# Kernel tuning notes

Hardware: AMD Instinct MI355X
Metric: run time of the kernel (lower is better)

The kernel has to match this reference:

```python
import jax, jax.numpy as jnp
import numpy as np

HIDDEN = 1024
NUM_HEADS = 16
HEAD_DIM = HIDDEN // NUM_HEADS
B, S = 2, 2048


def setup_inputs() -> dict:
    key = jax.random.key(0)
    ks = jax.random.split(key, 7)
    scale = 1.0 / np.sqrt(HIDDEN)
    return {
        "hidden_states": jax.random.normal(ks[0], (B, S, HIDDEN), dtype=jnp.float32),
        "attention_mask": jnp.ones((B, S), dtype=jnp.float32),
        "Wq": jax.random.normal(ks[1], (HIDDEN, HIDDEN), dtype=jnp.float32) * scale,
        "bq": jax.random.normal(ks[2], (HIDDEN,), dtype=jnp.float32) * 0.02,
        "Wk": jax.random.normal(ks[3], (HIDDEN, HIDDEN), dtype=jnp.float32) * scale,
        "bk": jax.random.normal(ks[4], (HIDDEN,), dtype=jnp.float32) * 0.02,
        "Wv": jax.random.normal(ks[5], (HIDDEN, HIDDEN), dtype=jnp.float32) * scale,
        "bv": jax.random.normal(ks[6], (HIDDEN,), dtype=jnp.float32) * 0.02,
    }


def reference(hidden_states, attention_mask, Wq, bq, Wk, bk, Wv, bv):
    # Linear projections (W stored [in, out], equivalent to torch Linear).
    q = hidden_states @ Wq + bq  # [B,S,H]
    k = hidden_states @ Wk + bk
    v = hidden_states @ Wv + bv

    def split_heads(x):  # [B,S,H] -> [B,nh,S,hd]
        return x.reshape(B, S, NUM_HEADS, HEAD_DIM).transpose(0, 2, 1, 3)

    q, k, v = split_heads(q), split_heads(k), split_heads(v)

    scores = jnp.einsum("bhqd,bhkd->bhqk", q, k) / jnp.sqrt(
        jnp.asarray(HEAD_DIM, dtype=q.dtype))
    min_val = jnp.finfo(scores.dtype).min
    ext_mask = (1.0 - attention_mask[:, None, None, :]) * min_val  # [B,1,1,S]
    scores = scores + ext_mask
    probs = jax.nn.softmax(scores, axis=-1)  # eval mode: no dropout
    ctx = jnp.einsum("bhqk,bhkd->bhqd", probs, v)
    ctx = ctx.transpose(0, 2, 1, 3).reshape(B, S, HIDDEN)
    return ctx
```

## Files before the change

kernel.cpp:

```cpp
#include <hip/hip_runtime.h>
#include <hip/hip_bf16.h>
#include <cstddef>
#include <cstdint>

#define HID 1024
#define NHEADS 16
#define HDIM 64
#define BATCH 2
#define SEQ 2048
#define MROWS (BATCH * SEQ)
#define BHT (BATCH * NHEADS)

typedef __attribute__((ext_vector_type(8))) short s8v;
typedef __attribute__((ext_vector_type(4))) float f4v;

__device__ __forceinline__ unsigned short f2bf(float x) {
    union { float f; unsigned int u; } c; c.f = x;
    return (unsigned short)((c.u + 0x7fffu + ((c.u >> 16) & 1u)) >> 16);
}
__device__ __forceinline__ unsigned int pkbf(float a, float b) {
    __hip_bfloat162 h = __float22bfloat162_rn(float2{a, b});
    union { __hip_bfloat162 v; unsigned int u; } c; c.v = h; return c.u;
}
__device__ __forceinline__ float bflo(unsigned int w) {
    union { unsigned int u; float f; } c; c.u = w << 16; return c.f;
}
__device__ __forceinline__ float bfhi(unsigned int w) {
    union { unsigned int u; float f; } c; c.u = w & 0xffff0000u; return c.f;
}

__device__ __forceinline__ void lds_load16(void* lds, const void* g) {
    __builtin_amdgcn_global_load_lds(
        (const __attribute__((address_space(1))) void*)g,
        (__attribute__((address_space(3))) void*)lds, 16, 0, 0);
}

__global__ __launch_bounds__(256) void conv_hs_kernel(
    const float* __restrict__ hs, unsigned short* __restrict__ Ah)
{
    const int idx = (blockIdx.x * 256 + threadIdx.x) * 4;
    float4 v = *(const float4*)&hs[idx];
    union { unsigned int w[2]; unsigned long long q; } pk;
    pk.w[0] = pkbf(v.x, v.y);
    pk.w[1] = pkbf(v.z, v.w);
    *(unsigned long long*)&Ah[idx] = pk.q;
}

__global__ __launch_bounds__(256) void conv_wt_kernel(
    const float* __restrict__ Wq, const float* __restrict__ Wk,
    const float* __restrict__ Wv, unsigned short* __restrict__ WTh)
{
    const int z = blockIdx.z;
    const float* W = (z == 0) ? Wq : (z == 1) ? Wk : Wv;
    unsigned short* th = WTh + (size_t)z * HID * HID;

    __shared__ float tile[64][65];
    const int t = threadIdx.x;
    const int kb = blockIdx.y * 64, nb = blockIdx.x * 64;
    const int c4 = (t & 15) * 4;
    const int r0 = t >> 4;

#pragma unroll
    for (int i = 0; i < 4; ++i) {
        int r = r0 + i * 16;
        float4 v = *(const float4*)&W[(size_t)(kb + r) * HID + nb + c4];
        tile[r][c4 + 0] = v.x; tile[r][c4 + 1] = v.y;
        tile[r][c4 + 2] = v.z; tile[r][c4 + 3] = v.w;
    }
    __syncthreads();
#pragma unroll
    for (int i = 0; i < 4; ++i) {
        int n = r0 + i * 16;
        union { unsigned int w[2]; unsigned long long q; } pk;
        pk.w[0] = pkbf(tile[c4 + 0][n], tile[c4 + 1][n]);
        pk.w[1] = pkbf(tile[c4 + 2][n], tile[c4 + 3][n]);
        *(unsigned long long*)&th[(size_t)(nb + n) * HID + kb + c4] = pk.q;
    }
}

#define GBM 128
#define GBN 128
#define QSCALE 0.18033688011112042f

__global__ __launch_bounds__(256) void qkv_mfma_kernel(
    const unsigned short* __restrict__ Ah, const unsigned short* __restrict__ WTh,
    const float* __restrict__ bq, const float* __restrict__ bk,
    const float* __restrict__ bv,
    unsigned short* __restrict__ Qg, unsigned short* __restrict__ Khi,
    unsigned short* __restrict__ VTg)
{
    const int z = blockIdx.z;
    const float* bias = (z == 0) ? bq : (z == 1) ? bk : bv;
    const unsigned short* Bh = WTh + (size_t)z * HID * HID;

    __shared__ unsigned short AS[GBM * 64];
    __shared__ unsigned short BS[GBN * 64];

    const int t = threadIdx.x;
    const int wave = t >> 6, lane = t & 63, quad = lane >> 4, l15 = lane & 15;
    const int sw = l15 & 7;
    const int wm = wave >> 1, wn = wave & 1;
    const int rowBase = blockIdx.x * GBM;
    const int colBase = blockIdx.y * GBN;

    const int srow8 = lane >> 3;
    const int sc    = lane & 7;

    f4v acc[4][4];
#pragma unroll
    for (int mf = 0; mf < 4; ++mf)
#pragma unroll
        for (int nf = 0; nf < 4; ++nf) acc[mf][nf] = (f4v){0.f, 0.f, 0.f, 0.f};

    for (int kt = 0; kt < HID / 64; ++kt) {
        const int k0 = kt * 64;
        __syncthreads();
#pragma unroll
        for (int it = 0; it < 4; ++it) {
            const int i = wave * 4 + it;
            const int row = i * 8 + srow8;
            const int gx = (sc ^ (row & 7)) * 8;
            lds_load16(&AS[i * 512], &Ah[(size_t)(rowBase + row) * HID + k0 + gx]);
            lds_load16(&BS[i * 512], &Bh[(size_t)(colBase + row) * HID + k0 + gx]);
        }
        __syncthreads();

#pragma unroll
        for (int kk = 0; kk < 2; ++kk) {
            s8v af[4], bf[4];
#pragma unroll
            for (int mf = 0; mf < 4; ++mf)
                af[mf] = *(const s8v*)&AS[(wm * 64 + mf * 16 + l15) * 64 + (((kk * 4 + quad) ^ sw) * 8)];
#pragma unroll
            for (int nf = 0; nf < 4; ++nf)
                bf[nf] = *(const s8v*)&BS[(wn * 64 + nf * 16 + l15) * 64 + (((kk * 4 + quad) ^ sw) * 8)];
#pragma unroll
            for (int mf = 0; mf < 4; ++mf)
#pragma unroll
                for (int nf = 0; nf < 4; ++nf)
                    acc[mf][nf] = __builtin_amdgcn_mfma_f32_16x16x32_bf16(af[mf], bf[nf], acc[mf][nf], 0, 0, 0);
        }
    }

#pragma unroll
    for (int nf = 0; nf < 4; ++nf) {
        const int n = colBase + wn * 64 + nf * 16 + l15;
        const float bb = bias[n];
        const int h = n >> 6, d = n & 63;
#pragma unroll
        for (int mf = 0; mf < 4; ++mf) {
            const int rw0 = rowBase + wm * 64 + mf * 16 + quad * 4;
            const int b = rw0 >> 11;
            const int s0 = rw0 & (SEQ - 1);
            float c[4];
#pragma unroll
            for (int r = 0; r < 4; ++r) c[r] = acc[mf][nf][r] + bb;
            if (z == 0) {
#pragma unroll
                for (int r = 0; r < 4; ++r) {
                    const size_t base = ((size_t)(b * NHEADS + h) * SEQ + s0 + r) * HDIM + d;
                    Qg[base] = f2bf(c[r] * QSCALE);
                }
            } else if (z == 1) {
#pragma unroll
                for (int r = 0; r < 4; ++r) {
                    const size_t base = ((size_t)(b * NHEADS + h) * SEQ + s0 + r) * HDIM + d;
                    Khi[base] = f2bf(c[r]);
                }
            } else {
                union { unsigned int w[2]; unsigned long long q; } pk;
                pk.w[0] = pkbf(c[0], c[1]);
                pk.w[1] = pkbf(c[2], c[3]);
                *(unsigned long long*)&VTg[((size_t)(b * NHEADS + h) * HDIM + d) * SEQ + s0] = pk.q;
            }
        }
    }
}

#define BC 64

__global__ __launch_bounds__(256, 2) void attn_mfma_kernel(
    const unsigned short* __restrict__ Qg, const unsigned short* __restrict__ Khi,
    const unsigned short* __restrict__ VTg,
    const float* __restrict__ mask, float* __restrict__ out)
{
    __shared__ unsigned short Kb[2][BC * HDIM];
    __shared__ unsigned short Vb[2][BC * HDIM];
    __shared__ unsigned short Pbuf[4][32 * BC];

    const int t = threadIdx.x;
    const int wave = t >> 6, lane = t & 63, quad = lane >> 4, l15 = lane & 15;
    const int sw = l15 & 7;
    const int bh = blockIdx.x, b = bh >> 4, h = bh & (NHEADS - 1);
    const int qbase = blockIdx.y * 128 + wave * 32;

    const size_t hb = (size_t)bh * SEQ * HDIM;
    const unsigned short* kbase = Khi + hb;
    const unsigned short* vbase = VTg + hb;
    const float* mrow = mask + b * SEQ;

    s8v qh[2][2];
#pragma unroll
    for (int qf = 0; qf < 2; ++qf)
#pragma unroll
        for (int ds = 0; ds < 2; ++ds) {
            size_t off = hb + (size_t)(qbase + qf * 16 + l15) * HDIM + ds * 32 + quad * 8;
            qh[qf][ds] = *(const s8v*)&Qg[off];
        }

    f4v oacc[2][4];
#pragma unroll
    for (int qf = 0; qf < 2; ++qf)
#pragma unroll
        for (int nf = 0; nf < 4; ++nf) oacc[qf][nf] = (f4v){0.f, 0.f, 0.f, 0.f};
    float l_r[2] = {0.f, 0.f};

    const int srow8 = lane >> 3;
    const int sc    = lane & 7;
    int koff[2], voff[2];
#pragma unroll
    for (int it = 0; it < 2; ++it) {
        const int row = (wave * 2 + it) * 8 + srow8;
        const int gx = (sc ^ (row & 7)) * 8;
        koff[it] = row * HDIM + gx;
        voff[it] = row * SEQ + gx;
    }

#pragma unroll
    for (int it = 0; it < 2; ++it) {
        const int i = wave * 2 + it;
        lds_load16(&Kb[0][i * 512], kbase + koff[it]);
        lds_load16(&Vb[0][i * 512], vbase + voff[it]);
    }
    __syncthreads();

    for (int kt = 0; kt < SEQ / BC; ++kt) {
        const int cur = kt & 1;
        if (kt + 1 < SEQ / BC) {
            const int nxt = cur ^ 1;
#pragma unroll
            for (int it = 0; it < 2; ++it) {
                const int i = wave * 2 + it;
                lds_load16(&Kb[nxt][i * 512], kbase + (kt + 1) * BC * HDIM + koff[it]);
                lds_load16(&Vb[nxt][i * 512], vbase + (kt + 1) * BC + voff[it]);
            }
        }
        float4 msv[4];
#pragma unroll
        for (int mf = 0; mf < 4; ++mf)
            msv[mf] = *(const float4*)&mrow[kt * BC + mf * 16 + quad * 4];

        f4v sacc[2][4];
#pragma unroll
        for (int qf = 0; qf < 2; ++qf)
#pragma unroll
            for (int mf = 0; mf < 4; ++mf) sacc[qf][mf] = (f4v){0.f, 0.f, 0.f, 0.f};
#pragma unroll
        for (int mf = 0; mf < 4; ++mf) {
#pragma unroll
            for (int ds = 0; ds < 2; ++ds) {
                s8v kh = *(const s8v*)&Kb[cur][(mf * 16 + l15) * HDIM + (((ds * 4 + quad) ^ sw) * 8)];
#pragma unroll
                for (int qf = 0; qf < 2; ++qf)
                    sacc[qf][mf] = __builtin_amdgcn_mfma_f32_16x16x32_bf16(kh, qh[qf][ds], sacc[qf][mf], 0, 0, 0);
            }
        }

#pragma unroll
        for (int qf = 0; qf < 2; ++qf) {
            float psum = 0.f;
            const int prow = (qf * 16 + l15) * BC;
#pragma unroll
            for (int mf = 0; mf < 4; ++mf) {
                const float* mp = (const float*)&msv[mf];
                float p0 = __builtin_amdgcn_exp2f(sacc[qf][mf][0]) * mp[0];
                float p1 = __builtin_amdgcn_exp2f(sacc[qf][mf][1]) * mp[1];
                float p2 = __builtin_amdgcn_exp2f(sacc[qf][mf][2]) * mp[2];
                float p3 = __builtin_amdgcn_exp2f(sacc[qf][mf][3]) * mp[3];
                union { unsigned int w[2]; unsigned long long q; } pk;
                pk.w[0] = pkbf(p0, p1);
                pk.w[1] = pkbf(p2, p3);
                psum += bflo(pk.w[0]) + bfhi(pk.w[0]) + bflo(pk.w[1]) + bfhi(pk.w[1]);
                const int c16 = (mf * 2 + (quad >> 1)) ^ sw;
                *(unsigned long long*)&Pbuf[wave][prow + c16 * 8 + (quad & 1) * 4] = pk.q;
            }
            l_r[qf] += psum;
        }

#pragma unroll
        for (int ks = 0; ks < 2; ++ks) {
            const int csw = ((ks * 4 + quad) ^ sw) * 8;
            s8v pa0 = *(const s8v*)&Pbuf[wave][(0 * 16 + l15) * BC + csw];
            s8v pa1 = *(const s8v*)&Pbuf[wave][(1 * 16 + l15) * BC + csw];
#pragma unroll
            for (int nf = 0; nf < 4; ++nf) {
                s8v vb = *(const s8v*)&Vb[cur][(nf * 16 + l15) * BC + csw];
                oacc[0][nf] = __builtin_amdgcn_mfma_f32_16x16x32_bf16(pa0, vb, oacc[0][nf], 0, 0, 0);
                oacc[1][nf] = __builtin_amdgcn_mfma_f32_16x16x32_bf16(pa1, vb, oacc[1][nf], 0, 0, 0);
            }
        }
        __syncthreads();
    }

#pragma unroll
    for (int qf = 0; qf < 2; ++qf) {
        float v = l_r[qf];
        v += __shfl_xor(v, 16);
        v += __shfl_xor(v, 32);
        float lv[4];
#pragma unroll
        for (int r = 0; r < 4; ++r)
            lv[r] = 1.0f / __shfl(v, quad * 4 + r);
#pragma unroll
        for (int nf = 0; nf < 4; ++nf)
#pragma unroll
            for (int r = 0; r < 4; ++r) {
                int q = qbase + qf * 16 + quad * 4 + r;
                int d = nf * 16 + l15;
                out[((size_t)b * SEQ + q) * HID + h * HDIM + d] = oacc[qf][nf][r] * lv[r];
            }
    }
}

extern "C" void kernel_launch(void* const* d_in, const int* in_sizes, int n_in,
                              void* d_out, int out_size, void* d_ws, size_t ws_size,
                              hipStream_t stream) {
    const float* hs   = (const float*)d_in[0];
    const float* mask = (const float*)d_in[1];
    const float* Wq   = (const float*)d_in[2];
    const float* bq   = (const float*)d_in[3];
    const float* Wk   = (const float*)d_in[4];
    const float* bk   = (const float*)d_in[5];
    const float* Wv   = (const float*)d_in[6];
    const float* bv   = (const float*)d_in[7];
    float* out = (float*)d_out;

    const size_t N = (size_t)MROWS * HID;
    unsigned short* Qg  = (unsigned short*)d_ws;
    unsigned short* Khi = Qg + N;
    unsigned short* VTg = Qg + 2 * N;
    unsigned short* Ah  = Qg + 3 * N;
    unsigned short* WTh = Qg + 4 * N;

    conv_hs_kernel<<<(MROWS * HID) / (256 * 4), 256, 0, stream>>>(hs, Ah);
    conv_wt_kernel<<<dim3(HID / 64, HID / 64, 3), 256, 0, stream>>>(Wq, Wk, Wv, WTh);

    dim3 g1(MROWS / GBM, HID / GBN, 3);
    qkv_mfma_kernel<<<g1, 256, 0, stream>>>(Ah, WTh, bq, bk, bv, Qg, Khi, VTg);

    dim3 g2(BHT, SEQ / 128);
    attn_mfma_kernel<<<g2, 256, 0, stream>>>(Qg, Khi, VTg, mask, out);
}
```

Measured before the change: 184.9 us.

## Fuse conversion kernels and double-buffer QKV GEMM with vectorized epilogue

Merges the hidden-state and weight conversion kernels into one launch, with wider 16-byte stores for the hidden-state cast. The QKV GEMM switches to a double-buffered K-tile of 32, so the next tile's global-to-LDS load overlaps the current tile's MFMAs. For Q and K it swaps the MFMA operand order so each lane holds four consecutive columns, which allows packed 8-byte stores instead of scalar 2-byte stores. The price is an unswizzled LDS layout that may cause bank conflicts, plus twice as many K iterations with a barrier in each.

```diff
diff --git a/kernel.cpp b/kernel.cpp
--- a/kernel.cpp
+++ b/kernel.cpp
@@ -35,46 +35,51 @@
         (__attribute__((address_space(3))) void*)lds, 16, 0, 0);
 }
 
-__global__ __launch_bounds__(256) void conv_hs_kernel(
-    const float* __restrict__ hs, unsigned short* __restrict__ Ah)
+__global__ __launch_bounds__(256) void conv_fused_kernel(
+    const float* __restrict__ hs,
+    const float* __restrict__ Wq, const float* __restrict__ Wk,
+    const float* __restrict__ Wv,
+    unsigned short* __restrict__ Ah, unsigned short* __restrict__ WTh)
 {
-    const int idx = (blockIdx.x * 256 + threadIdx.x) * 4;
-    float4 v = *(const float4*)&hs[idx];
-    union { unsigned int w[2]; unsigned long long q; } pk;
-    pk.w[0] = pkbf(v.x, v.y);
-    pk.w[1] = pkbf(v.z, v.w);
-    *(unsigned long long*)&Ah[idx] = pk.q;
-}
-
-__global__ __launch_bounds__(256) void conv_wt_kernel(
-    const float* __restrict__ Wq, const float* __restrict__ Wk,
-    const float* __restrict__ Wv, unsigned short* __restrict__ WTh)
-{
-    const int z = blockIdx.z;
-    const float* W = (z == 0) ? Wq : (z == 1) ? Wk : Wv;
-    unsigned short* th = WTh + (size_t)z * HID * HID;
-
-    __shared__ float tile[64][65];
-    const int t = threadIdx.x;
-    const int kb = blockIdx.y * 64, nb = blockIdx.x * 64;
-    const int c4 = (t & 15) * 4;
-    const int r0 = t >> 4;
-
-#pragma unroll
-    for (int i = 0; i < 4; ++i) {
-        int r = r0 + i * 16;
-        float4 v = *(const float4*)&W[(size_t)(kb + r) * HID + nb + c4];
-        tile[r][c4 + 0] = v.x; tile[r][c4 + 1] = v.y;
-        tile[r][c4 + 2] = v.z; tile[r][c4 + 3] = v.w;
-    }
-    __syncthreads();
-#pragma unroll
-    for (int i = 0; i < 4; ++i) {
-        int n = r0 + i * 16;
-        union { unsigned int w[2]; unsigned long long q; } pk;
-        pk.w[0] = pkbf(tile[c4 + 0][n], tile[c4 + 1][n]);
-        pk.w[1] = pkbf(tile[c4 + 2][n], tile[c4 + 3][n]);
-        *(unsigned long long*)&th[(size_t)(nb + n) * HID + kb + c4] = pk.q;
+    if (blockIdx.x < 2048) {
+        const int idx = (blockIdx.x * 256 + threadIdx.x) * 8;
+        float4 v0 = *(const float4*)&hs[idx];
+        float4 v1 = *(const float4*)&hs[idx + 4];
+        union { unsigned int w[4]; } pk;
+        pk.w[0] = pkbf(v0.x, v0.y);
+        pk.w[1] = pkbf(v0.z, v0.w);
+        pk.w[2] = pkbf(v1.x, v1.y);
+        pk.w[3] = pkbf(v1.z, v1.w);
+        *(uint4*)&Ah[idx] = *(uint4*)&pk;
+    } else {
+        const int bid = blockIdx.x - 2048;
+        const int z = bid >> 8;
+        const int rem = bid & 255;
+        const float* W = (z == 0) ? Wq : (z == 1) ? Wk : Wv;
+        unsigned short* th = WTh + (size_t)z * HID * HID;
+
+        __shared__ float tile[64][65];
+        const int t = threadIdx.x;
+        const int kb = (rem >> 4) * 64, nb = (rem & 15) * 64;
+        const int c4 = (t & 15) * 4;
+        const int r0 = t >> 4;
+
+#pragma unroll
+        for (int i = 0; i < 4; ++i) {
+            int r = r0 + i * 16;
+            float4 v = *(const float4*)&W[(size_t)(kb + r) * HID + nb + c4];
+            tile[r][c4 + 0] = v.x; tile[r][c4 + 1] = v.y;
+            tile[r][c4 + 2] = v.z; tile[r][c4 + 3] = v.w;
+        }
+        __syncthreads();
+#pragma unroll
+        for (int i = 0; i < 4; ++i) {
+            int n = r0 + i * 16;
+            union { unsigned int w[2]; unsigned long long q; } pk;
+            pk.w[0] = pkbf(tile[c4 + 0][n], tile[c4 + 1][n]);
+            pk.w[1] = pkbf(tile[c4 + 2][n], tile[c4 + 3][n]);
+            *(unsigned long long*)&th[(size_t)(nb + n) * HID + kb + c4] = pk.q;
+        }
     }
 }
 
@@ -93,18 +98,24 @@
     const float* bias = (z == 0) ? bq : (z == 1) ? bk : bv;
     const unsigned short* Bh = WTh + (size_t)z * HID * HID;
 
-    __shared__ unsigned short AS[GBM * 64];
-    __shared__ unsigned short BS[GBN * 64];
+    __shared__ unsigned short AS[2][GBM * 32];
+    __shared__ unsigned short BS[2][GBN * 32];
 
     const int t = threadIdx.x;
     const int wave = t >> 6, lane = t & 63, quad = lane >> 4, l15 = lane & 15;
-    const int sw = l15 & 7;
     const int wm = wave >> 1, wn = wave & 1;
     const int rowBase = blockIdx.x * GBM;
     const int colBase = blockIdx.y * GBN;
 
-    const int srow8 = lane >> 3;
-    const int sc    = lane & 7;
+    const int srow = lane >> 2;
+    const int sc8  = (lane & 3) * 8;
+    size_t goffA[2], goffB[2];
+#pragma unroll
+    for (int it = 0; it < 2; ++it) {
+        const int rA = wave * 32 + it * 16;
+        goffA[it] = (size_t)(rowBase + rA + srow) * HID + sc8;
+        goffB[it] = (size_t)(colBase + rA + srow) * HID + sc8;
+    }
 
     f4v acc[4][4];
 #pragma unroll
@@ -112,66 +123,83 @@
 #pragma unroll
         for (int nf = 0; nf < 4; ++nf) acc[mf][nf] = (f4v){0.f, 0.f, 0.f, 0.f};
 
-    for (int kt = 0; kt < HID / 64; ++kt) {
-        const int k0 = kt * 64;
-        __syncthreads();
-#pragma unroll
-        for (int it = 0; it < 4; ++it) {
-            const int i = wave * 4 + it;
-            const int row = i * 8 + srow8;
-            const int gx = (sc ^ (row & 7)) * 8;
-            lds_load16(&AS[i * 512], &Ah[(size_t)(rowBase + row) * HID + k0 + gx]);
-            lds_load16(&BS[i * 512], &Bh[(size_t)(colBase + row) * HID + k0 + gx]);
-        }
-        __syncthreads();
-
-#pragma unroll
-        for (int kk = 0; kk < 2; ++kk) {
-            s8v af[4], bf[4];
-#pragma unroll
-            for (int mf = 0; mf < 4; ++mf)
-                af[mf] = *(const s8v*)&AS[(wm * 64 + mf * 16 + l15) * 64 + (((kk * 4 + quad) ^ sw) * 8)];
-#pragma unroll
-            for (int nf = 0; nf < 4; ++nf)
-                bf[nf] = *(const s8v*)&BS[(wn * 64 + nf * 16 + l15) * 64 + (((kk * 4 + quad) ^ sw) * 8)];
+#pragma unroll
+    for (int it = 0; it < 2; ++it) {
+        const int rA = wave * 32 + it * 16;
+        lds_load16(&AS[0][rA * 32], &Ah[goffA[it]]);
+        lds_load16(&BS[0][rA * 32], &Bh[goffB[it]]);
+    }
+    __syncthreads();
+
+    for (int kt = 0; kt < HID / 32; ++kt) {
+        const int cur = kt & 1;
+        if (kt + 1 < HID / 32) {
+            const int nxt = cur ^ 1;
+            const int k0 = (kt + 1) * 32;
+#pragma unroll
+            for (int it = 0; it < 2; ++it) {
+                const int rA = wave * 32 + it * 16;
+                lds_load16(&AS[nxt][rA * 32], &Ah[goffA[it] + k0]);
+                lds_load16(&BS[nxt][rA * 32], &Bh[goffB[it] + k0]);
+            }
+        }
+        s8v af[4], bf[4];
+#pragma unroll
+        for (int mf = 0; mf < 4; ++mf)
+            af[mf] = *(const s8v*)&AS[cur][(wm * 64 + mf * 16 + l15) * 32 + quad * 8];
+#pragma unroll
+        for (int nf = 0; nf < 4; ++nf)
+            bf[nf] = *(const s8v*)&BS[cur][(wn * 64 + nf * 16 + l15) * 32 + quad * 8];
+        if (z == 2) {
 #pragma unroll
             for (int mf = 0; mf < 4; ++mf)
 #pragma unroll
                 for (int nf = 0; nf < 4; ++nf)
                     acc[mf][nf] = __builtin_amdgcn_mfma_f32_16x16x32_bf16(af[mf], bf[nf], acc[mf][nf], 0, 0, 0);
-        }
-    }
-
-#pragma unroll
-    for (int nf = 0; nf < 4; ++nf) {
-        const int n = colBase + wn * 64 + nf * 16 + l15;
-        const float bb = bias[n];
-        const int h = n >> 6, d = n & 63;
-#pragma unroll
-        for (int mf = 0; mf < 4; ++mf) {
-            const int rw0 = rowBase + wm * 64 + mf * 16 + quad * 4;
-            const int b = rw0 >> 11;
-            const int s0 = rw0 & (SEQ - 1);
-            float c[4];
-#pragma unroll
-            for (int r = 0; r < 4; ++r) c[r] = acc[mf][nf][r] + bb;
-            if (z == 0) {
-#pragma unroll
-                for (int r = 0; r < 4; ++r) {
-                    const size_t base = ((size_t)(b * NHEADS + h) * SEQ + s0 + r) * HDIM + d;
-                    Qg[base] = f2bf(c[r] * QSCALE);
-                }
-            } else if (z == 1) {
-#pragma unroll
-                for (int r = 0; r < 4; ++r) {
-                    const size_t base = ((size_t)(b * NHEADS + h) * SEQ + s0 + r) * HDIM + d;
-                    Khi[base] = f2bf(c[r]);
-                }
-            } else {
+        } else {
+#pragma unroll
+            for (int mf = 0; mf < 4; ++mf)
+#pragma unroll
+                for (int nf = 0; nf < 4; ++nf)
+                    acc[mf][nf] = __builtin_amdgcn_mfma_f32_16x16x32_bf16(bf[nf], af[mf], acc[mf][nf], 0, 0, 0);
+        }
+        __syncthreads();
+    }
+
+    if (z == 2) {
+#pragma unroll
+        for (int nf = 0; nf < 4; ++nf) {
+            const int n = colBase + wn * 64 + nf * 16 + l15;
+            const float bb = bias[n];
+            const int h = n >> 6, d = n & 63;
+#pragma unroll
+            for (int mf = 0; mf < 4; ++mf) {
+                const int rw0 = rowBase + wm * 64 + mf * 16 + quad * 4;
+                const int b = rw0 >> 11;
+                const int s0 = rw0 & (SEQ - 1);
                 union { unsigned int w[2]; unsigned long long q; } pk;
-                pk.w[0] = pkbf(c[0], c[1]);
-                pk.w[1] = pkbf(c[2], c[3]);
+                pk.w[0] = pkbf(acc[mf][nf][0] + bb, acc[mf][nf][1] + bb);
+                pk.w[1] = pkbf(acc[mf][nf][2] + bb, acc[mf][nf][3] + bb);
                 *(unsigned long long*)&VTg[((size_t)(b * NHEADS + h) * HDIM + d) * SEQ + s0] = pk.q;
+            }
+        }
+    } else {
+        unsigned short* outp = (z == 0) ? Qg : Khi;
+        const float scale = (z == 0) ? QSCALE : 1.0f;
+#pragma unroll
+        for (int nf = 0; nf < 4; ++nf) {
+            const int n0 = colBase + wn * 64 + nf * 16 + quad * 4;
+            const float4 bb = *(const float4*)&bias[n0];
+            const int h = n0 >> 6, d0 = n0 & 63;
+#pragma unroll
+            for (int mf = 0; mf < 4; ++mf) {
+                const int rw = rowBase + wm * 64 + mf * 16 + l15;
+                const int b = rw >> 11;
+                const int ss = rw & (SEQ - 1);
+                union { unsigned int w[2]; unsigned long long q; } pk;
+                pk.w[0] = pkbf((acc[mf][nf][0] + bb.x) * scale, (acc[mf][nf][1] + bb.y) * scale);
+                pk.w[1] = pkbf((acc[mf][nf][2] + bb.z) * scale, (acc[mf][nf][3] + bb.w) * scale);
+                *(unsigned long long*)&outp[((size_t)(b * NHEADS + h) * SEQ + ss) * HDIM + d0] = pk.q;
             }
         }
     }
@@ -342,8 +370,7 @@
     unsigned short* Ah  = Qg + 3 * N;
     unsigned short* WTh = Qg + 4 * N;
 
-    conv_hs_kernel<<<(MROWS * HID) / (256 * 4), 256, 0, stream>>>(hs, Ah);
-    conv_wt_kernel<<<dim3(HID / 64, HID / 64, 3), 256, 0, stream>>>(Wq, Wk, Wv, WTh);
+    conv_fused_kernel<<<2048 + 768, 256, 0, stream>>>(hs, Wq, Wk, Wv, Ah, WTh);
 
     dim3 g1(MROWS / GBM, HID / GBN, 3);
     qkv_mfma_kernel<<<g1, 256, 0, stream>>>(Ah, WTh, bq, bk, bv, Qg, Khi, VTg);
```

Result: slower. 199.3 us (+7.8%).

## Merge conversion kernels and shrink QKV GEMM tile for higher occupancy

Applied to the files above, without the earlier changes.

Merges the hidden-state bf16 conversion and the weight transpose-conversion into one launch, and widens the hidden-state conversion to 8 elements per thread. The QKV GEMM tile drops from 128x128 to 64x128 with each wave owning a 64x32 slice, doubling the grid and requesting 5 blocks per CU. Global load offsets are precomputed outside the k loop. The aim is less launch overhead and better latency hiding, at the cost of lower per-block data reuse and more redundant B-tile loads.

```diff
diff --git a/kernel.cpp b/kernel.cpp
--- a/kernel.cpp
+++ b/kernel.cpp
@@ -35,54 +35,59 @@
         (__attribute__((address_space(3))) void*)lds, 16, 0, 0);
 }
 
-__global__ __launch_bounds__(256) void conv_hs_kernel(
-    const float* __restrict__ hs, unsigned short* __restrict__ Ah)
+__global__ __launch_bounds__(256) void conv_fused_kernel(
+    const float* __restrict__ hs,
+    const float* __restrict__ Wq, const float* __restrict__ Wk,
+    const float* __restrict__ Wv,
+    unsigned short* __restrict__ Ah, unsigned short* __restrict__ WTh)
 {
-    const int idx = (blockIdx.x * 256 + threadIdx.x) * 4;
-    float4 v = *(const float4*)&hs[idx];
-    union { unsigned int w[2]; unsigned long long q; } pk;
-    pk.w[0] = pkbf(v.x, v.y);
-    pk.w[1] = pkbf(v.z, v.w);
-    *(unsigned long long*)&Ah[idx] = pk.q;
-}
-
-__global__ __launch_bounds__(256) void conv_wt_kernel(
-    const float* __restrict__ Wq, const float* __restrict__ Wk,
-    const float* __restrict__ Wv, unsigned short* __restrict__ WTh)
-{
-    const int z = blockIdx.z;
-    const float* W = (z == 0) ? Wq : (z == 1) ? Wk : Wv;
-    unsigned short* th = WTh + (size_t)z * HID * HID;
-
-    __shared__ float tile[64][65];
-    const int t = threadIdx.x;
-    const int kb = blockIdx.y * 64, nb = blockIdx.x * 64;
-    const int c4 = (t & 15) * 4;
-    const int r0 = t >> 4;
-
-#pragma unroll
-    for (int i = 0; i < 4; ++i) {
-        int r = r0 + i * 16;
-        float4 v = *(const float4*)&W[(size_t)(kb + r) * HID + nb + c4];
-        tile[r][c4 + 0] = v.x; tile[r][c4 + 1] = v.y;
-        tile[r][c4 + 2] = v.z; tile[r][c4 + 3] = v.w;
-    }
-    __syncthreads();
-#pragma unroll
-    for (int i = 0; i < 4; ++i) {
-        int n = r0 + i * 16;
-        union { unsigned int w[2]; unsigned long long q; } pk;
-        pk.w[0] = pkbf(tile[c4 + 0][n], tile[c4 + 1][n]);
-        pk.w[1] = pkbf(tile[c4 + 2][n], tile[c4 + 3][n]);
-        *(unsigned long long*)&th[(size_t)(nb + n) * HID + kb + c4] = pk.q;
-    }
-}
-
-#define GBM 128
-#define GBN 128
+    if (blockIdx.x < 2048) {
+        const int idx = (blockIdx.x * 256 + threadIdx.x) * 8;
+        float4 v0 = *(const float4*)&hs[idx];
+        float4 v1 = *(const float4*)&hs[idx + 4];
+        union { unsigned int w[4]; } pk;
+        pk.w[0] = pkbf(v0.x, v0.y);
+        pk.w[1] = pkbf(v0.z, v0.w);
+        pk.w[2] = pkbf(v1.x, v1.y);
+        pk.w[3] = pkbf(v1.z, v1.w);
+        *(uint4*)&Ah[idx] = *(uint4*)&pk;
+    } else {
+        const int bid = blockIdx.x - 2048;
+        const int z = bid >> 8;
+        const int rem = bid & 255;
+        const float* W = (z == 0) ? Wq : (z == 1) ? Wk : Wv;
+        unsigned short* th = WTh + (size_t)z * HID * HID;
+
+        __shared__ float tile[64][65];
+        const int t = threadIdx.x;
+        const int kb = (rem >> 4) * 64, nb = (rem & 15) * 64;
+        const int c4 = (t & 15) * 4;
+        const int r0 = t >> 4;
+
+#pragma unroll
+        for (int i = 0; i < 4; ++i) {
+            int r = r0 + i * 16;
+            float4 v = *(const float4*)&W[(size_t)(kb + r) * HID + nb + c4];
+            tile[r][c4 + 0] = v.x; tile[r][c4 + 1] = v.y;
+            tile[r][c4 + 2] = v.z; tile[r][c4 + 3] = v.w;
+        }
+        __syncthreads();
+#pragma unroll
+        for (int i = 0; i < 4; ++i) {
+            int n = r0 + i * 16;
+            union { unsigned int w[2]; unsigned long long q; } pk;
+            pk.w[0] = pkbf(tile[c4 + 0][n], tile[c4 + 1][n]);
+            pk.w[1] = pkbf(tile[c4 + 2][n], tile[c4 + 3][n]);
+            *(unsigned long long*)&th[(size_t)(nb + n) * HID + kb + c4] = pk.q;
+        }
+    }
+}
+
+#define QBM 64
+#define QBN 128
 #define QSCALE 0.18033688011112042f
 
-__global__ __launch_bounds__(256) void qkv_mfma_kernel(
+__global__ __launch_bounds__(256, 5) void qkv_mfma_kernel(
     const unsigned short* __restrict__ Ah, const unsigned short* __restrict__ WTh,
     const float* __restrict__ bq, const float* __restrict__ bk,
     const float* __restrict__ bv,
@@ -93,63 +98,73 @@
     const float* bias = (z == 0) ? bq : (z == 1) ? bk : bv;
     const unsigned short* Bh = WTh + (size_t)z * HID * HID;
 
-    __shared__ unsigned short AS[GBM * 64];
-    __shared__ unsigned short BS[GBN * 64];
+    __shared__ unsigned short AS[QBM * 64];
+    __shared__ unsigned short BS[QBN * 64];
 
     const int t = threadIdx.x;
     const int wave = t >> 6, lane = t & 63, quad = lane >> 4, l15 = lane & 15;
     const int sw = l15 & 7;
-    const int wm = wave >> 1, wn = wave & 1;
-    const int rowBase = blockIdx.x * GBM;
-    const int colBase = blockIdx.y * GBN;
+    const int rowBase = blockIdx.x * QBM;
+    const int colBase = blockIdx.y * QBN;
 
     const int srow8 = lane >> 3;
     const int sc    = lane & 7;
 
-    f4v acc[4][4];
+    size_t goffA[2], goffB[4];
+#pragma unroll
+    for (int it = 0; it < 2; ++it) {
+        const int row = (wave * 2 + it) * 8 + srow8;
+        goffA[it] = (size_t)(rowBase + row) * HID + (sc ^ (row & 7)) * 8;
+    }
+#pragma unroll
+    for (int it = 0; it < 4; ++it) {
+        const int row = (wave * 4 + it) * 8 + srow8;
+        goffB[it] = (size_t)(colBase + row) * HID + (sc ^ (row & 7)) * 8;
+    }
+
+    f4v acc[4][2];
 #pragma unroll
     for (int mf = 0; mf < 4; ++mf)
 #pragma unroll
-        for (int nf = 0; nf < 4; ++nf) acc[mf][nf] = (f4v){0.f, 0.f, 0.f, 0.f};
+        for (int nf = 0; nf < 2; ++nf) acc[mf][nf] = (f4v){0.f, 0.f, 0.f, 0.f};
 
     for (int kt = 0; kt < HID / 64; ++kt) {
         const int k0 = kt * 64;
         __syncthreads();
 #pragma unroll
-        for (int it = 0; it < 4; ++it) {
-            const int i = wave * 4 + it;
-            const int row = i * 8 + srow8;
-            const int gx = (sc ^ (row & 7)) * 8;
-            lds_load16(&AS[i * 512], &Ah[(size_t)(rowBase + row) * HID + k0 + gx]);
-            lds_load16(&BS[i * 512], &Bh[(size_t)(colBase + row) * HID + k0 + gx]);
-        }
+        for (int it = 0; it < 2; ++it)
+            lds_load16(&AS[(wave * 2 + it) * 512], &Ah[goffA[it] + k0]);
+#pragma unroll
+        for (int it = 0; it < 4; ++it)
+            lds_load16(&BS[(wave * 4 + it) * 512], &Bh[goffB[it] + k0]);
         __syncthreads();
 
 #pragma unroll
         for (int kk = 0; kk < 2; ++kk) {
-            s8v af[4], bf[4];
+            const int csw = ((kk * 4 + quad) ^ sw) * 8;
+            s8v af[4], bf[2];
 #pragma unroll
             for (int mf = 0; mf < 4; ++mf)
-                af[mf] = *(const s8v*)&AS[(wm * 64 + mf * 16 + l15) * 64 + (((kk * 4 + quad) ^ sw) * 8)];
-#pragma unroll
-            for (int nf = 0; nf < 4; ++nf)
-                bf[nf] = *(const s8v*)&BS[(wn * 64 + nf * 16 + l15) * 64 + (((kk * 4 + quad) ^ sw) * 8)];
+                af[mf] = *(const s8v*)&AS[(mf * 16 + l15) * 64 + csw];
+#pragma unroll
+            for (int nf = 0; nf < 2; ++nf)
+                bf[nf] = *(const s8v*)&BS[(wave * 32 + nf * 16 + l15) * 64 + csw];
 #pragma unroll
             for (int mf = 0; mf < 4; ++mf)
 #pragma unroll
-                for (int nf = 0; nf < 4; ++nf)
+                for (int nf = 0; nf < 2; ++nf)
                     acc[mf][nf] = __builtin_amdgcn_mfma_f32_16x16x32_bf16(af[mf], bf[nf], acc[mf][nf], 0, 0, 0);
         }
     }
 
 #pragma unroll
-    for (int nf = 0; nf < 4; ++nf) {
-        const int n = colBase + wn * 64 + nf * 16 + l15;
+    for (int nf = 0; nf < 2; ++nf) {
+        const int n = colBase + wave * 32 + nf * 16 + l15;
         const float bb = bias[n];
         const int h = n >> 6, d = n & 63;
 #pragma unroll
         for (int mf = 0; mf < 4; ++mf) {
-            const int rw0 = rowBase + wm * 64 + mf * 16 + quad * 4;
+            const int rw0 = rowBase + mf * 16 + quad * 4;
             const int b = rw0 >> 11;
             const int s0 = rw0 & (SEQ - 1);
             float c[4];
@@ -157,16 +172,12 @@
             for (int r = 0; r < 4; ++r) c[r] = acc[mf][nf][r] + bb;
             if (z == 0) {
 #pragma unroll
-                for (int r = 0; r < 4; ++r) {
-                    const size_t base = ((size_t)(b * NHEADS + h) * SEQ + s0 + r) * HDIM + d;
-                    Qg[base] = f2bf(c[r] * QSCALE);
-                }
+                for (int r = 0; r < 4; ++r)
+                    Qg[((size_t)(b * NHEADS + h) * SEQ + s0 + r) * HDIM + d] = f2bf(c[r] * QSCALE);
             } else if (z == 1) {
 #pragma unroll
-                for (int r = 0; r < 4; ++r) {
-                    const size_t base = ((size_t)(b * NHEADS + h) * SEQ + s0 + r) * HDIM + d;
-                    Khi[base] = f2bf(c[r]);
-                }
+                for (int r = 0; r < 4; ++r)
+                    Khi[((size_t)(b * NHEADS + h) * SEQ + s0 + r) * HDIM + d] = f2bf(c[r]);
             } else {
                 union { unsigned int w[2]; unsigned long long q; } pk;
                 pk.w[0] = pkbf(c[0], c[1]);
@@ -342,10 +353,9 @@
     unsigned short* Ah  = Qg + 3 * N;
     unsigned short* WTh = Qg + 4 * N;
 
-    conv_hs_kernel<<<(MROWS * HID) / (256 * 4), 256, 0, stream>>>(hs, Ah);
-    conv_wt_kernel<<<dim3(HID / 64, HID / 64, 3), 256, 0, stream>>>(Wq, Wk, Wv, WTh);
-
-    dim3 g1(MROWS / GBM, HID / GBN, 3);
+    conv_fused_kernel<<<2048 + 768, 256, 0, stream>>>(hs, Wq, Wk, Wv, Ah, WTh);
+
+    dim3 g1(MROWS / QBM, HID / QBN, 3);
     qkv_mfma_kernel<<<g1, 256, 0, stream>>>(Ah, WTh, bq, bk, bv, Qg, Khi, VTg);
 
     dim3 g2(BHT, SEQ / 128);
```

Result: faster. 180.1 us (-2.6%).
